# Optimization experiments

Measured on AMD Instinct MI355X. Metric: run time of the kernel, lower is better.

Reference implementation:

```python
import jax, jax.numpy as jnp
import numpy as np
from jax import lax

B, C_VIS, C_GRAPH, C_OUT, H, W, K = 8, 256, 256, 256, 96, 96, 3


def conv2d(x, w, b):
    # x: [B,Cin,H,W], w: [Cout,Cin,K,K], SAME padding (pad = K//2)
    y = lax.conv_general_dilated(x, w, window_strides=(1, 1), padding='SAME',
                                 dimension_numbers=('NCHW', 'OIHW', 'NCHW'))
    return y + b[None, :, None, None]


def setup_inputs() -> dict:
    key = jax.random.key(0)
    ks = jax.random.split(key, 12)
    scale_v = 1.0 / np.sqrt(C_VIS * K * K)
    scale_g = 1.0 / np.sqrt(C_GRAPH * K * K)
    scale_o = 1.0 / np.sqrt(C_OUT * K * K)
    return {
        'feats': jax.random.normal(ks[0], (B, C_VIS, H, W), jnp.float32),
        'graph_feature': jax.random.normal(ks[1], (B, C_GRAPH, H, W), jnp.float32),
        'wq': jax.random.normal(ks[2], (C_OUT, C_GRAPH, K, K), jnp.float32) * scale_g,
        'bq': jax.random.normal(ks[3], (C_OUT,), jnp.float32) * 0.01,
        'wk': jax.random.normal(ks[4], (C_OUT, C_VIS, K, K), jnp.float32) * scale_v,
        'bk': jax.random.normal(ks[5], (C_OUT,), jnp.float32) * 0.01,
        'wv': jax.random.normal(ks[6], (C_OUT, C_VIS, K, K), jnp.float32) * scale_v,
        'bv': jax.random.normal(ks[7], (C_OUT,), jnp.float32) * 0.01,
        'wo': jax.random.normal(ks[8], (C_OUT, C_OUT, K, K), jnp.float32) * scale_o,
        'bo': jax.random.normal(ks[9], (C_OUT,), jnp.float32) * 0.01,
    }


def reference(feats, graph_feature, wq, bq, wk, bk, wv, bv, wo, bo):
    q = conv2d(graph_feature, wq, bq)  # [B,C,H,W]
    k = conv2d(feats, wk, bk)          # [B,C,H,W]
    v = conv2d(feats, wv, bv)          # [B,C,H,W]
    # attention over rows: attn[b,c,i,j] = sum_w q[b,c,i,w] * k[b,c,j,w]
    scale = 1.0 / jnp.sqrt(jnp.asarray(k.shape[-1], q.dtype))
    attn = jnp.einsum('bchw,bcgw->bchg', q, k) * scale  # [B,C,H,H]
    attn = jax.nn.softmax(attn, axis=-1)
    fused = jnp.einsum('bchg,bcgw->bchw', attn, v)      # [B,C,H,W]
    return conv2d(fused, wo, bo)
```

## Files before the change

### kernel.cpp

```cpp
#include <hip/hip_runtime.h>
#include <hip/hip_bf16.h>

constexpr int BATCH = 8;
constexpr int CH    = 256;
constexpr int H     = 96;
constexpr int W     = 96;
constexpr int HW    = H * W;
constexpr long PLANE_ELEMS = (long)BATCH * CH * HW;
constexpr int PAD   = 98;

typedef short  bf16x8_t __attribute__((ext_vector_type(8)));
typedef float  f32x4_t  __attribute__((ext_vector_type(4)));

__device__ inline uint pk2_bf16(float a, float b) {
  ushort lo = __bfloat16_as_ushort(__float2bfloat16(a));
  ushort hi = __bfloat16_as_ushort(__float2bfloat16(b));
  return (uint)lo | ((uint)hi << 16);
}

#define WAITVM(N) asm volatile("s_waitcnt vmcnt(" #N ")" ::: "memory")

__device__ __forceinline__ void gl_lds16(const ushort* g, ushort* l) {
  __builtin_amdgcn_global_load_lds(
      (const __attribute__((address_space(1))) void*)g,
      (__attribute__((address_space(3))) void*)l, 16, 0, 0);
}

__global__ __launch_bounds__(256) void prep_wb(
    const float* __restrict__ s0, const float* __restrict__ s1,
    const float* __restrict__ s2, const float* __restrict__ s3,
    ushort* __restrict__ d0, ushort* __restrict__ d1,
    ushort* __restrict__ d2, ushort* __restrict__ d3,
    ushort* __restrict__ p0, ushort* __restrict__ p1)
{
  if (blockIdx.x < 9216) {
    const int t = blockIdx.x / 2304;
    const int idx = (blockIdx.x % 2304) * 256 + threadIdx.x;
    const float* s = (t == 0) ? s0 : (t == 1) ? s1 : (t == 2) ? s2 : s3;
    ushort* d      = (t == 0) ? d0 : (t == 1) ? d1 : (t == 2) ? d2 : d3;
    const int e   = idx & 7;
    const int lg  = (idx >> 3) & 3;
    const int l15 = (idx >> 5) & 15;
    const int q   = (idx >> 9) & 15;
    const int cc  = (idx >> 13) & 7;
    const int tap = idx >> 16;
    const int co  = q * 16 + l15;
    const int ci  = cc * 32 + lg * 8 + e;
    d[idx] = __bfloat16_as_ushort(__float2bfloat16(s[(co * 256 + ci) * 9 + tap]));
    return;
  }
  const int bb = blockIdx.x - 9216;
  const int ub = bb % 49;
  const int b  = (bb / 49) & 7;
  ushort* p = (bb >= 392) ? p1 : p0;
  const int u = ub * 256 + threadIdx.x;
  if (u >= 12416) return;
  int y, x, cu;
  if (u < 6272)      { y = (u < 3136) ? 0 : 97; int r = u % 3136; x = r >> 5; cu = r & 31; }
  else               { int r = u - 6272; x = (r < 3072) ? 0 : 97; int r2 = r % 3072; y = 1 + (r2 >> 5); cu = r2 & 31; }
  int4 z = make_int4(0, 0, 0, 0);
  *(int4*)&p[(((long)b * PAD + y) * PAD + x) * 256 + cu * 8] = z;
}

__global__ __launch_bounds__(256) void nchw_f32_to_nhwc_bf16_2(
    const float* __restrict__ in0, const float* __restrict__ in1,
    ushort* __restrict__ out0, ushort* __restrict__ out1)
{
  __shared__ float t[32][33];
  const int tid = threadIdx.x;
  const int p0 = blockIdx.x * 32;
  const int c0 = blockIdx.y * 32;
  const int ts = blockIdx.z >> 3;
  const int b  = blockIdx.z & 7;
  const float* in = ts ? in1 : in0;
  ushort* out     = ts ? out1 : out0;
  const int tp = tid & 31, tc8 = tid >> 5;
#pragma unroll
  for (int i = 0; i < 4; ++i) {
    int c = tc8 + i * 8;
    t[c][tp] = in[((long)(b * 256 + c0 + c)) * HW + p0 + tp];
  }
  __syncthreads();
  const int wc = tid & 31, wp8 = tid >> 5;
#pragma unroll
  for (int i = 0; i < 4; ++i) {
    int p = p0 + wp8 + i * 8;
    int y = p / 96, x = p % 96;
    out[(((long)b * PAD + y + 1) * PAD + x + 1) * 256 + c0 + wc] =
        __bfloat16_as_ushort(__float2bfloat16(t[wc][wp8 + i * 8]));
  }
}

__global__ __launch_bounds__(256) void nchw_bf16_to_nhwc_bf16(
    const ushort* __restrict__ in, ushort* __restrict__ out)
{
  __shared__ ushort t[32][34];
  const int tid = threadIdx.x;
  const int p0 = blockIdx.x * 32;
  const int c0 = blockIdx.y * 32;
  const int b  = blockIdx.z;
  const int tp = tid & 31, tc8 = tid >> 5;
#pragma unroll
  for (int i = 0; i < 4; ++i) {
    int c = tc8 + i * 8;
    t[c][tp] = in[((long)(b * 256 + c0 + c)) * HW + p0 + tp];
  }
  __syncthreads();
  const int wc = tid & 31, wp8 = tid >> 5;
#pragma unroll
  for (int i = 0; i < 4; ++i) {
    int p = p0 + wp8 + i * 8;
    int y = p / 96, x = p % 96;
    out[(((long)b * PAD + y + 1) * PAD + x + 1) * 256 + c0 + wc] = t[wc][wp8 + i * 8];
  }
}

template <int NT, typename OutT>
__global__ __launch_bounds__(256, 2) void conv3x3_mfma(
    const ushort* pin0, const ushort* pin1,
    const ushort* w0, const ushort* w1, const ushort* w2,
    const float* bias0, const float* bias1, const float* bias2,
    OutT* o0, OutT* o1, OutT* o2)
{
  const int tid  = threadIdx.x;
  const int lane = tid & 63;
  const int wv   = tid >> 6;
  const int wm   = wv & 1;
  const int wn   = wv >> 1;
  const int l15  = lane & 15;
  const int lg   = lane >> 4;

  const int nwg = NT * 768;
  const int cpx = nwg >> 3;
  const int swz = ((int)blockIdx.x & 7) * cpx + ((int)blockIdx.x >> 3);
  const int t    = swz / 768;
  const int rest = swz % 768;
  const ushort* pin = (t == 2) ? pin1 : pin0;
  const ushort* wt  = (t == 0) ? w0 : (t == 1) ? w1 : w2;
  const float* bias = (t == 0) ? bias0 : (t == 1) ? bias1 : bias2;
  OutT* out         = (t == 0) ? o0 : (t == 1) ? o1 : o2;

  const int cox = rest & 1;
  const int yb  = (rest >> 1) % 48;
  const int b   = (rest >> 1) / 48;
  const int co0 = cox * 128;
  const int y0  = yb * 2;
  const int coq = cox * 8 + wm * 4;
  const int alo = (l15 * 4 + lg) << 3;

  __shared__ ushort sIn[2][1568 * 8];

  f32x4_t acc[4][6];
#pragma unroll
  for (int m = 0; m < 4; ++m)
#pragma unroll
    for (int n = 0; n < 6; ++n)
      acc[m][n] = (f32x4_t){0.f, 0.f, 0.f, 0.f};

  auto issueIN = [&](int cc) {
    const int ci0 = cc * 32;
    const int ubase = wv * 392;
#pragma unroll
    for (int it = 0; it < 7; ++it) {
      int lo = it * 64 + lane;
      if (lo < 392) {
        int u  = ubase + lo;
        int q  = u >> 2;
        int g  = u & 3;
        int xx = q % 98, rr = q / 98;
        int ug = g ^ ((xx + (xx >> 2)) & 3);
        const ushort* src = pin + (((long)(b * PAD + y0 + rr)) * PAD + xx) * 256 + ci0 + ug * 8;
        ushort* dst = (ushort*)((char*)&sIn[cc & 1][0] + (long)u * 16);
        gl_lds16(src, dst);
      }
    }
  };

  auto glda = [&](int tap, int cc, int m) -> bf16x8_t {
    return *(const bf16x8_t*)&wt[(((tap * 8 + cc) * 16 + coq + m) << 9) + alo];
  };

  bf16x8_t a0[4], a1[4], a2[4];
  bf16x8_t bbA[6], bbB[6];

#define ISSUE_A(CC, TAP, AR)                \
  if ((CC) < 8) {                           \
    AR[0] = glda((TAP), (CC), 0);           \
    AR[1] = glda((TAP), (CC), 1);           \
    AR[2] = glda((TAP), (CC), 2);           \
    AR[3] = glda((TAP), (CC), 3);           \
  }

#define LOAD_B(BB, DY, DX)                                                  \
  {                                                                         \
    const int s__    = l15 + (DX);                                          \
    const int boff__ = (lg ^ ((s__ + (s__ >> 2)) & 3)) << 4;                \
    const int rr__   = wn + (DY);                                           \
    _Pragma("unroll")                                                       \
    for (int n = 0; n < 6; ++n)                                             \
      BB[n] = *(const bf16x8_t*)(Bb + ((rr__ * 98 + n * 16 + s__) << 6) + boff__); \
  }

#define DO_MFMA(BB, AR)                                                     \
  __builtin_amdgcn_s_setprio(1);                                            \
  _Pragma("unroll")                                                         \
  for (int m = 0; m < 4; ++m)                                               \
    _Pragma("unroll")                                                       \
    for (int n = 0; n < 6; ++n)                                             \
      acc[m][n] = __builtin_amdgcn_mfma_f32_16x16x32_bf16(                  \
          AR[m], BB[n], acc[m][n], 0, 0, 0);                                \
  __builtin_amdgcn_s_setprio(0);

  issueIN(0);
  __builtin_amdgcn_sched_barrier(0);
  ISSUE_A(0, 0, a0);
  ISSUE_A(0, 1, a1);
  __builtin_amdgcn_sched_barrier(0);
  WAITVM(8);
  __builtin_amdgcn_s_barrier();
  __builtin_amdgcn_sched_barrier(0);

#pragma unroll 1
  for (int c = 0; c < 8; ++c) {
    const char* Bb = (const char*)&sIn[c & 1][0];
    if (c < 7) issueIN(c + 1);
    __builtin_amdgcn_sched_barrier(0);
    LOAD_B(bbA, 0, 0);
    ISSUE_A(c, 2, a2)      LOAD_B(bbB, 0, 1)  DO_MFMA(bbA, a0)
    ISSUE_A(c, 3, a0)      LOAD_B(bbA, 0, 2)  DO_MFMA(bbB, a1)
    ISSUE_A(c, 4, a1)      LOAD_B(bbB, 1, 0)  DO_MFMA(bbA, a2)
    ISSUE_A(c, 5, a2)      LOAD_B(bbA, 1, 1)  DO_MFMA(bbB, a0)
    ISSUE_A(c, 6, a0)      LOAD_B(bbB, 1, 2)  DO_MFMA(bbA, a1)
    ISSUE_A(c, 7, a1)      LOAD_B(bbA, 2, 0)  DO_MFMA(bbB, a2)
    ISSUE_A(c, 8, a2)      LOAD_B(bbB, 2, 1)  DO_MFMA(bbA, a0)
    ISSUE_A(c + 1, 0, a0)  LOAD_B(bbA, 2, 2)  DO_MFMA(bbB, a1)
    ISSUE_A(c + 1, 1, a1)                     DO_MFMA(bbA, a2)
    __builtin_amdgcn_sched_barrier(0);
    if (c < 7) { WAITVM(36); } else { WAITVM(0); }
    __builtin_amdgcn_s_barrier();
    __builtin_amdgcn_sched_barrier(0);
  }
#undef ISSUE_A
#undef LOAD_B
#undef DO_MFMA

  if constexpr (sizeof(OutT) == 2) {
    char* sE = (char*)&sIn[0][0];
#pragma unroll
    for (int h = 0; h < 2; ++h) {
      if (wm == h) {
#pragma unroll
        for (int m = 0; m < 4; ++m)
#pragma unroll
          for (int r = 0; r < 4; ++r) {
            const int col = m * 16 + lg * 4 + r;
            const float bv = bias[co0 + h * 64 + col];
#pragma unroll
            for (int n = 0; n < 6; ++n) {
              *(ushort*)(sE + col * 400 + (wn * 96 + n * 16 + l15) * 2) =
                  __bfloat16_as_ushort(__float2bfloat16(acc[m][n][r] + bv));
            }
          }
      }
      __syncthreads();
#pragma unroll
      for (int it = 0; it < 7; ++it) {
        int u = it * 256 + tid;
        if (u < 1600) {
          int co = u / 25, ru = u % 25;
          if (ru < 24) {
            int4 v = *(const int4*)(sE + co * 400 + ru * 16);
            int e0 = ru * 8;
            int yy = y0 + (e0 >= 96);
            int x  = e0 - (e0 >= 96 ? 96 : 0);
            *(int4*)&out[(((long)(b * 256 + co0 + h * 64 + co)) * 96 + yy) * 96 + x] = v;
          }
        }
      }
      __syncthreads();
    }
  } else {
    char* sE = (char*)&sIn[0][0];
#pragma unroll
    for (int h = 0; h < 2; ++h) {
      if (wm == h) {
#pragma unroll
        for (int m = 0; m < 4; ++m)
#pragma unroll
          for (int r = 0; r < 4; ++r) {
            const int col = m * 16 + lg * 4 + r;
            const float bv = bias[co0 + h * 64 + col];
#pragma unroll
            for (int n = 0; n < 6; ++n) {
              *(float*)(sE + (col * 196 + wn * 96 + n * 16 + l15) * 4) =
                  acc[m][n][r] + bv;
            }
          }
      }
      __syncthreads();
#pragma unroll
      for (int it = 0; it < 12; ++it) {
        int u = it * 256 + tid;
        int co = u / 48, ru = u % 48;
        int4 v = *(const int4*)(sE + (co * 196 + ru * 4) * 4);
        int e0 = ru * 4;
        int yy = y0 + (e0 >= 96);
        int x  = e0 - (e0 >= 96 ? 96 : 0);
        *(int4*)&out[(((long)(b * 256 + co0 + h * 64 + co)) * 96 + yy) * 96 + x] = v;
      }
      __syncthreads();
    }
  }
}

constexpr int APITCH = 104;

__global__ __launch_bounds__(384, 3) void attn_mfma(
    const ushort* __restrict__ q,
    const ushort* __restrict__ k,
    const ushort* __restrict__ v,
    ushort* __restrict__ outf)
{
  __shared__ ushort sK [96 * APITCH];
  __shared__ ushort sVt[96 * APITCH];
  __shared__ ushort sP [6 * 16 * APITCH];

  const int tid  = threadIdx.x;
  const int lane = tid & 63;
  const int wv   = tid >> 6;
  const int l15  = lane & 15;
  const int lg   = lane >> 4;
  const long plane = (long)blockIdx.x * HW;

  for (int u = tid; u < 1152; u += 384) {
    int j = u / 12, c8 = u % 12;
    *(int4*)&sK[j * APITCH + c8 * 8] = *(const int4*)&k[plane + j * 96 + c8 * 8];
  }
  for (int u = tid; u < 1152; u += 384) {
    int j = u % 96, c8 = u / 96;
    ushort tmp[8];
    *(int4*)tmp = *(const int4*)&v[plane + j * 96 + c8 * 8];
#pragma unroll
    for (int e = 0; e < 8; ++e)
      sVt[(c8 * 8 + e) * APITCH + j] = tmp[e];
  }
  __syncthreads();

  const int i0 = wv * 16;

  bf16x8_t qf[3];
#pragma unroll
  for (int ks = 0; ks < 3; ++ks)
    qf[ks] = *(const bf16x8_t*)&q[plane + (i0 + l15) * 96 + ks * 32 + lg * 8];

  f32x4_t s[6];
#pragma unroll
  for (int jt = 0; jt < 6; ++jt) s[jt] = (f32x4_t){0.f, 0.f, 0.f, 0.f};
#pragma unroll
  for (int jt = 0; jt < 6; ++jt)
#pragma unroll
    for (int ks = 0; ks < 3; ++ks) {
      bf16x8_t kf = *(const bf16x8_t*)&sK[(jt * 16 + l15) * APITCH + ks * 32 + lg * 8];
      s[jt] = __builtin_amdgcn_mfma_f32_16x16x32_bf16(kf, qf[ks], s[jt], 0, 0, 0);
    }

  const float sc = 0.10206207261596575f;
  float m = -3.0e38f;
#pragma unroll
  for (int jt = 0; jt < 6; ++jt)
#pragma unroll
    for (int r = 0; r < 4; ++r) m = fmaxf(m, s[jt][r]);
  m = fmaxf(m, __shfl_xor(m, 16));
  m = fmaxf(m, __shfl_xor(m, 32));

  float p[6][4];
  float sum = 0.f;
#pragma unroll
  for (int jt = 0; jt < 6; ++jt)
#pragma unroll
    for (int r = 0; r < 4; ++r) {
      float e = __expf((s[jt][r] - m) * sc);
      p[jt][r] = e;
      sum += e;
    }
  sum += __shfl_xor(sum, 16);
  sum += __shfl_xor(sum, 32);
  const float inv = 1.f / sum;

  ushort* myP = &sP[wv * 16 * APITCH];
#pragma unroll
  for (int jt = 0; jt < 6; ++jt) {
    *(uint*)&myP[l15 * APITCH + jt * 16 + lg * 4] =
        pk2_bf16(p[jt][0] * inv, p[jt][1] * inv);
    *(uint*)&myP[l15 * APITCH + jt * 16 + lg * 4 + 2] =
        pk2_bf16(p[jt][2] * inv, p[jt][3] * inv);
  }

  bf16x8_t pf[3];
#pragma unroll
  for (int ks = 0; ks < 3; ++ks)
    pf[ks] = *(const bf16x8_t*)&myP[l15 * APITCH + ks * 32 + lg * 8];

  f32x4_t o[6];
#pragma unroll
  for (int wt = 0; wt < 6; ++wt) o[wt] = (f32x4_t){0.f, 0.f, 0.f, 0.f};
#pragma unroll
  for (int wt = 0; wt < 6; ++wt)
#pragma unroll
    for (int ks = 0; ks < 3; ++ks) {
      bf16x8_t vf = *(const bf16x8_t*)&sVt[(wt * 16 + l15) * APITCH + ks * 32 + lg * 8];
      o[wt] = __builtin_amdgcn_mfma_f32_16x16x32_bf16(pf[ks], vf, o[wt], 0, 0, 0);
    }

#pragma unroll
  for (int wt = 0; wt < 6; ++wt)
#pragma unroll
    for (int r = 0; r < 4; ++r) {
      int i = i0 + lg * 4 + r;
      outf[plane + i * 96 + wt * 16 + l15] =
          __bfloat16_as_ushort(__float2bfloat16(o[wt][r]));
    }
}

extern "C" void kernel_launch(void* const* d_in, const int* in_sizes, int n_in,
                              void* d_out, int out_size, void* d_ws, size_t ws_size,
                              hipStream_t stream) {
  (void)in_sizes; (void)n_in; (void)out_size; (void)ws_size;

  const float* feats = (const float*)d_in[0];
  const float* graph = (const float*)d_in[1];
  const float* wq    = (const float*)d_in[2];
  const float* bq    = (const float*)d_in[3];
  const float* wk    = (const float*)d_in[4];
  const float* bk    = (const float*)d_in[5];
  const float* wv    = (const float*)d_in[6];
  const float* bv    = (const float*)d_in[7];
  const float* wo    = (const float*)d_in[8];
  const float* bo    = (const float*)d_in[9];
  float* out = (float*)d_out;

  char* ws = (char*)d_ws;
  const long planeB   = PLANE_ELEMS * 2;
  const long pinElems = (long)BATCH * PAD * PAD * 256;
  ushort* qb   = (ushort*)ws;
  ushort* kb   = (ushort*)(ws + planeB);
  ushort* vb   = (ushort*)(ws + 2 * planeB);
  ushort* pinF = (ushort*)(ws + 3 * planeB);
  ushort* pinG = pinF + pinElems;
  ushort* wtq  = pinG + pinElems;
  ushort* wtk  = wtq + 9 * 256 * 256;
  ushort* wtv  = wtk + 9 * 256 * 256;
  ushort* wto  = wtv + 9 * 256 * 256;

  dim3 tgrid2(HW / 32, CH / 32, 2 * BATCH);
  dim3 tgrid (HW / 32, CH / 32, BATCH);
  dim3 agrid (BATCH * CH);

  prep_wb<<<9216 + 784, 256, 0, stream>>>(wq, wk, wv, wo, wtq, wtk, wtv, wto,
                                          pinF, pinG);

  nchw_f32_to_nhwc_bf16_2<<<tgrid2, 256, 0, stream>>>(feats, graph, pinF, pinG);

  conv3x3_mfma<3, ushort><<<3 * 768, 256, 0, stream>>>(
      pinF, pinG, wtk, wtv, wtq, bk, bv, bq, kb, vb, qb);

  attn_mfma<<<agrid, 384, 0, stream>>>(qb, kb, vb, qb);

  nchw_bf16_to_nhwc_bf16<<<tgrid, 256, 0, stream>>>(qb, pinF);

  conv3x3_mfma<1, float><<<768, 256, 0, stream>>>(
      pinF, pinF, wto, wto, wto, bo, bo, bo, out, out, out);
}
```

Measured before the change: 469.4 us.

## Unroll conv channel loop by two with double-buffered A and mid-chunk input prefetch

Restructures the 3x3 conv MFMA main loop. It processes two channel chunks per iteration with fixed LDS buffer pointers, cuts the weight register triple-buffer to a double buffer, and moves the next-chunk input LDS prefetch to the middle of the tap sequence. Weight prefetch now runs only one tap ahead, so VGPR pressure drops and occupancy may rise. The trade-off is less latency hiding for the global weight loads, and the prologue now waits for all loads to finish.

```diff
diff --git a/kernel.cpp b/kernel.cpp
--- a/kernel.cpp
+++ b/kernel.cpp
@@ -180,8 +180,10 @@
     return *(const bf16x8_t*)&wt[(((tap * 8 + cc) * 16 + coq + m) << 9) + alo];
   };
 
-  bf16x8_t a0[4], a1[4], a2[4];
+  bf16x8_t a0[4], a1[4];
   bf16x8_t bbA[6], bbB[6];
+  const char* Bb0 = (const char*)&sIn[0][0];
+  const char* Bb1 = (const char*)&sIn[1][0];
 
 #define ISSUE_A(CC, TAP, AR)                \
   if ((CC) < 8) {                           \
@@ -191,14 +193,14 @@
     AR[3] = glda((TAP), (CC), 3);           \
   }
 
-#define LOAD_B(BB, DY, DX)                                                  \
+#define LOAD_B(BB, BP, DY, DX)                                              \
   {                                                                         \
     const int s__    = l15 + (DX);                                          \
     const int boff__ = (lg ^ ((s__ + (s__ >> 2)) & 3)) << 4;                \
     const int rr__   = wn + (DY);                                           \
     _Pragma("unroll")                                                       \
     for (int n = 0; n < 6; ++n)                                             \
-      BB[n] = *(const bf16x8_t*)(Bb + ((rr__ * 98 + n * 16 + s__) << 6) + boff__); \
+      BB[n] = *(const bf16x8_t*)(BP + ((rr__ * 98 + n * 16 + s__) << 6) + boff__); \
   }
 
 #define DO_MFMA(BB, AR)                                                     \
@@ -212,31 +214,45 @@
   __builtin_amdgcn_s_setprio(0);
 
   issueIN(0);
-  __builtin_amdgcn_sched_barrier(0);
   ISSUE_A(0, 0, a0);
-  ISSUE_A(0, 1, a1);
-  __builtin_amdgcn_sched_barrier(0);
-  WAITVM(8);
+  WAITVM(0);
   __builtin_amdgcn_s_barrier();
   __builtin_amdgcn_sched_barrier(0);
 
 #pragma unroll 1
-  for (int c = 0; c < 8; ++c) {
-    const char* Bb = (const char*)&sIn[c & 1][0];
-    if (c < 7) issueIN(c + 1);
+  for (int k = 0; k < 4; ++k) {
+    const int c = 2 * k;
+    const int d = c + 1;
+    LOAD_B(bbA, Bb0, 0, 0);
+    ISSUE_A(c, 1, a1)  LOAD_B(bbB, Bb0, 0, 1)  DO_MFMA(bbA, a0)
+    ISSUE_A(c, 2, a0)  LOAD_B(bbA, Bb0, 0, 2)  DO_MFMA(bbB, a1)
+    ISSUE_A(c, 3, a1)  LOAD_B(bbB, Bb0, 1, 0)  DO_MFMA(bbA, a0)
+    ISSUE_A(c, 4, a0)
+    issueIN(d);
+    LOAD_B(bbA, Bb0, 1, 1)  DO_MFMA(bbB, a1)
+    ISSUE_A(c, 5, a1)  LOAD_B(bbB, Bb0, 1, 2)  DO_MFMA(bbA, a0)
+    ISSUE_A(c, 6, a0)  LOAD_B(bbA, Bb0, 2, 0)  DO_MFMA(bbB, a1)
+    ISSUE_A(c, 7, a1)  LOAD_B(bbB, Bb0, 2, 1)  DO_MFMA(bbA, a0)
+    ISSUE_A(c, 8, a0)  LOAD_B(bbA, Bb0, 2, 2)  DO_MFMA(bbB, a1)
+    ISSUE_A(d, 0, a1)  DO_MFMA(bbA, a0)
     __builtin_amdgcn_sched_barrier(0);
-    LOAD_B(bbA, 0, 0);
-    ISSUE_A(c, 2, a2)      LOAD_B(bbB, 0, 1)  DO_MFMA(bbA, a0)
-    ISSUE_A(c, 3, a0)      LOAD_B(bbA, 0, 2)  DO_MFMA(bbB, a1)
-    ISSUE_A(c, 4, a1)      LOAD_B(bbB, 1, 0)  DO_MFMA(bbA, a2)
-    ISSUE_A(c, 5, a2)      LOAD_B(bbA, 1, 1)  DO_MFMA(bbB, a0)
-    ISSUE_A(c, 6, a0)      LOAD_B(bbB, 1, 2)  DO_MFMA(bbA, a1)
-    ISSUE_A(c, 7, a1)      LOAD_B(bbA, 2, 0)  DO_MFMA(bbB, a2)
-    ISSUE_A(c, 8, a2)      LOAD_B(bbB, 2, 1)  DO_MFMA(bbA, a0)
-    ISSUE_A(c + 1, 0, a0)  LOAD_B(bbA, 2, 2)  DO_MFMA(bbB, a1)
-    ISSUE_A(c + 1, 1, a1)                     DO_MFMA(bbA, a2)
+    WAITVM(4);
+    __builtin_amdgcn_s_barrier();
     __builtin_amdgcn_sched_barrier(0);
-    if (c < 7) { WAITVM(36); } else { WAITVM(0); }
+    LOAD_B(bbB, Bb1, 0, 0);
+    ISSUE_A(d, 1, a0)  LOAD_B(bbA, Bb1, 0, 1)  DO_MFMA(bbB, a1)
+    ISSUE_A(d, 2, a1)  LOAD_B(bbB, Bb1, 0, 2)  DO_MFMA(bbA, a0)
+    ISSUE_A(d, 3, a0)  LOAD_B(bbA, Bb1, 1, 0)  DO_MFMA(bbB, a1)
+    ISSUE_A(d, 4, a1)
+    if (k < 3) issueIN(d + 1);
+    LOAD_B(bbB, Bb1, 1, 1)  DO_MFMA(bbA, a0)
+    ISSUE_A(d, 5, a0)  LOAD_B(bbA, Bb1, 1, 2)  DO_MFMA(bbB, a1)
+    ISSUE_A(d, 6, a1)  LOAD_B(bbB, Bb1, 2, 0)  DO_MFMA(bbA, a0)
+    ISSUE_A(d, 7, a0)  LOAD_B(bbA, Bb1, 2, 1)  DO_MFMA(bbB, a1)
+    ISSUE_A(d, 8, a1)  LOAD_B(bbB, Bb1, 2, 2)  DO_MFMA(bbA, a0)
+    ISSUE_A(d + 1, 0, a0)  DO_MFMA(bbB, a1)
+    __builtin_amdgcn_sched_barrier(0);
+    if (k < 3) { WAITVM(4); } else { WAITVM(0); }
     __builtin_amdgcn_s_barrier();
     __builtin_amdgcn_sched_barrier(0);
   }
```

New measurement: 508.2 us. 8.3% more time.
